# Kernel tuning notes

Measured on AMD Instinct MI355X. Metric: run time of the kernel, lower is better.

The kernel has to match this reference:

```python
import jax, jax.numpy as jnp
import numpy as np

N0, N1, N2 = 100000, 20000, 4000
E1, E2 = 500000, 100000
F_IN, H, C = 512, 512, 10


def setup_inputs() -> dict:
    key = jax.random.key(0)
    ks = jax.random.split(key, 16)
    s = 0.02  # weight scale
    return {
        "x": jax.random.normal(ks[0], (N0, F_IN), jnp.float32),
        "src1": jax.random.randint(ks[1], (E1,), 0, N0),
        "dst1": jax.random.randint(ks[2], (E1,), 0, N1),
        "src2": jax.random.randint(ks[3], (E2,), 0, N1),
        "dst2": jax.random.randint(ks[4], (E2,), 0, N2),
        "Wrel1": jax.random.normal(ks[5], (F_IN, H), jnp.float32) * s,
        "brel1": jax.random.normal(ks[6], (H,), jnp.float32) * s,
        "Wroot1": jax.random.normal(ks[7], (F_IN, H), jnp.float32) * s,
        "Wrel2": jax.random.normal(ks[8], (H, H), jnp.float32) * s,
        "brel2": jax.random.normal(ks[9], (H,), jnp.float32) * s,
        "Wroot2": jax.random.normal(ks[10], (H, H), jnp.float32) * s,
        "Wlin": jax.random.normal(ks[11], (H, H), jnp.float32) * s,
        "blin": jax.random.normal(ks[12], (H,), jnp.float32) * s,
        "Whead": jax.random.normal(ks[13], (H, C), jnp.float32) * s,
        "bhead": jax.random.normal(ks[14], (C,), jnp.float32) * s,
    }


def graph_conv(x_src, x_tgt, src, dst, n_tgt, Wrel, brel, Wroot):
    # PyG GraphConv, aggr='add': lin_rel(sum_j x_src[src_j] -> dst) + lin_root(x_tgt)
    agg = jax.ops.segment_sum(x_src[src], dst, num_segments=n_tgt)
    return agg @ Wrel + brel + x_tgt @ Wroot


def reference(x, src1, dst1, src2, dst2,
              Wrel1, brel1, Wroot1, Wrel2, brel2, Wroot2,
              Wlin, blin, Whead, bhead):
    # Layer 1: [N0, F] -> [N1, H]
    h = graph_conv(x, x[:N1], src1, dst1, N1, Wrel1, brel1, Wroot1)
    h = jax.nn.relu(h)  # dropout is identity in eval mode
    # Layer 2: [N1, H] -> [N2, H]
    h2 = graph_conv(h, h[:N2], src2, dst2, N2, Wrel2, brel2, Wroot2)
    # Dense head
    return (h2 @ Wlin + blin) @ Whead + bhead
```

## Files before the change

kernel.cpp:

```cpp
#include <hip/hip_runtime.h>
#include <hip/hip_bf16.h>
#include <cstdint>


static constexpr int N0 = 100000;
static constexpr int N1 = 20000;
static constexpr int N2 = 4000;
static constexpr int HH = 512;
static constexpr int C  = 10;
static constexpr int M1PAD = 20096;
static constexpr int SLOT = 64;

using frag  = __attribute__((ext_vector_type(8))) short;
using f32x4 = __attribute__((ext_vector_type(4))) float;

__device__ inline float bf2f(unsigned short u) {
    unsigned t = ((unsigned)u) << 16; float f; __builtin_memcpy(&f, &t, 4); return f;
}
__device__ inline unsigned short f2bf(float f) {
    unsigned u; __builtin_memcpy(&u, &f, 4);
    u += 0x7FFFu + ((u >> 16) & 1u);
    return (unsigned short)(u >> 16);
}
__device__ inline void gld16(const void* g, void* l) {
    __builtin_amdgcn_global_load_lds((const __attribute__((address_space(1))) void*)g,
                                     (__attribute__((address_space(3))) void*)l,
                                     16, 0, 0);
}

__global__ __launch_bounds__(256)
void prep1_k(const int* __restrict__ src1, const int* __restrict__ dst1,
             const int* __restrict__ src2, const int* __restrict__ dst2,
             int* __restrict__ cnt1, int* __restrict__ cnt2,
             int* __restrict__ eidx1, int* __restrict__ eidx2,
             int E1, int E2,
             const float* __restrict__ x, unsigned short* __restrict__ xb,
             const float* __restrict__ Wrel1, const float* __restrict__ Wroot1,
             unsigned short* __restrict__ Wt,
             const float* __restrict__ Wlin, const float* __restrict__ Whead,
             float* __restrict__ P1,
             int epb) {
    __shared__ float sh[5120];
    int b = blockIdx.x;
    const int tid = threadIdx.x;
    if (b < 20) {
        for (int i = tid; i < HH * C; i += 256) sh[i] = Whead[i];
        __syncthreads();
        int g = b * 256 + tid;
        int k = g / C, c = g % C;
        const float4* rp = (const float4*)(Wlin + (size_t)k * HH);
        float a0 = 0.f, a1 = 0.f, a2 = 0.f, a3 = 0.f;
#pragma unroll 4
        for (int j = 0; j < HH / 4; ++j) {
            float4 v = rp[j];
            int j4 = j * 4;
            a0 += v.x * sh[(j4    ) * C + c];
            a1 += v.y * sh[(j4 + 1) * C + c];
            a2 += v.z * sh[(j4 + 2) * C + c];
            a3 += v.w * sh[(j4 + 3) * C + c];
        }
        P1[g] = (a0 + a1) + (a2 + a3);
        return;
    }
    b -= 20;
    if (b < 512) {
        int z = b >> 8, rem = b & 255;
        int bx = (rem & 15) * 32, by = (rem >> 4) * 32;
        const float* W = z ? Wroot1 : Wrel1;
        unsigned short* O = Wt + (size_t)z * HH * HH;
        int tx = tid & 31, ty = tid >> 5;
#pragma unroll
        for (int i = 0; i < 4; ++i)
            sh[(ty + i * 8) * 33 + tx] = W[(size_t)(by + ty + i * 8) * HH + bx + tx];
        __syncthreads();
#pragma unroll
        for (int i = 0; i < 4; ++i)
            O[(size_t)(bx + ty + i * 8) * HH + by + tx] = f2bf(sh[tx * 33 + ty + i * 8]);
        return;
    }
    b -= 512;
    {
        int eg = b * epb + tid;
        bool hasE = (tid < epb) && (eg < E1 + E2);
        if (hasE) {
            if (eg < E1) {
                int d = dst1[eg];
                int pos = atomicAdd(&cnt1[d], 1);
                if (pos < SLOT) eidx1[d * SLOT + pos] = src1[eg];
            } else {
                int g2 = eg - E1;
                int d = dst2[g2];
                int pos = atomicAdd(&cnt2[d], 1);
                if (pos < SLOT) eidx2[d * SLOT + pos] = src2[g2];
            }
        }
        int g = b * 256 + tid;
        const float4* p = (const float4*)x + (size_t)g * 4;
        float4 v0 = p[0], v1 = p[1], v2 = p[2], v3 = p[3];
        unsigned short t[16] = {f2bf(v0.x), f2bf(v0.y), f2bf(v0.z), f2bf(v0.w),
                                f2bf(v1.x), f2bf(v1.y), f2bf(v1.z), f2bf(v1.w),
                                f2bf(v2.x), f2bf(v2.y), f2bf(v2.z), f2bf(v2.w),
                                f2bf(v3.x), f2bf(v3.y), f2bf(v3.z), f2bf(v3.w)};
        uint4* o = (uint4*)(xb + (size_t)g * 16);
        o[0] = ((const uint4*)t)[0];
        o[1] = ((const uint4*)t)[1];
    }
}

__global__ __launch_bounds__(1024)
void prep2_k(const float* __restrict__ Wrel2, const float* __restrict__ Wroot2,
             const float* __restrict__ P1,
             const float* __restrict__ brel2, const float* __restrict__ blin,
             const float* __restrict__ Whead, const float* __restrict__ bhead,
             float* __restrict__ W2aT, float* __restrict__ W2bT,
             float* __restrict__ bout) {
    __shared__ float fsh[5120];
    int blk = blockIdx.x;
    int t = threadIdx.x;
    if (blk < 10) {
        for (int i = t; i < HH * C; i += 1024) fsh[i] = P1[i];
        __syncthreads();
        int z = blk >= 5;
        int g = (blk - z * 5) * 1024 + t;
        if (g < HH * C) {
            const float* W = z ? Wroot2 : Wrel2;
            float* O = z ? W2bT : W2aT;
            int k = g / C, c = g % C;
            const float4* rp = (const float4*)(W + (size_t)k * HH);
            float a0 = 0.f, a1 = 0.f, a2 = 0.f, a3 = 0.f;
#pragma unroll 4
            for (int j = 0; j < HH / 4; ++j) {
                float4 v = rp[j];
                int j4 = j * 4;
                a0 += v.x * fsh[(j4    ) * C + c];
                a1 += v.y * fsh[(j4 + 1) * C + c];
                a2 += v.z * fsh[(j4 + 2) * C + c];
                a3 += v.w * fsh[(j4 + 3) * C + c];
            }
            O[c * HH + k] = (a0 + a1) + (a2 + a3);
        }
        return;
    }
    {
        float pr[C];
#pragma unroll
        for (int c = 0; c < C; ++c) pr[c] = 0.f;
        if (t < HH) {
            float br = brel2[t], bl = blin[t];
            const float* p1r = P1 + (size_t)t * C;
            const float* whr = Whead + (size_t)t * C;
#pragma unroll
            for (int c = 0; c < C; ++c) pr[c] = br * p1r[c] + bl * whr[c];
        }
#pragma unroll
        for (int c = 0; c < C; ++c)
#pragma unroll
            for (int off = 32; off; off >>= 1) pr[c] += __shfl_xor(pr[c], off);
        int wv = t >> 6, ln = t & 63;
        if (ln == 0)
#pragma unroll
            for (int c = 0; c < C; ++c) fsh[wv * C + c] = pr[c];
        __syncthreads();
        if (t < C) {
            float acc = bhead[t];
#pragma unroll
            for (int w = 0; w < 16; ++w) acc += fsh[w * C + t];
            bout[t] = acc;
        }
    }
}

__global__ __launch_bounds__(256)
void agg_bf16_k(const unsigned short* __restrict__ x, const int* __restrict__ cnt,
                const int* __restrict__ eidx, unsigned short* __restrict__ out, int n) {
    int node = blockIdx.x * 4 + (threadIdx.x >> 6);
    if (node >= n) return;
    int l = threadIdx.x & 63;
    int deg = min(cnt[node], SLOT);
    const int* ep = eidx + (size_t)node * SLOT;
    int acc[8] = {};
    int i = 0;
    for (; i + 8 <= deg; i += 8) {
        uint4 v[8];
#pragma unroll
        for (int u = 0; u < 8; ++u)
            v[u] = *(const uint4*)(x + (size_t)ep[i + u] * HH + l * 8);
#pragma unroll
        for (int u = 0; u < 8; ++u) {
            const unsigned short* pv = (const unsigned short*)&v[u];
#pragma unroll
            for (int j = 0; j < 8; ++j) acc[j] += (int)(bf2f(pv[j]) * 1048576.0f);
        }
    }
    for (; i < deg; ++i) {
        uint4 a = *(const uint4*)(x + (size_t)ep[i] * HH + l * 8);
        const unsigned short* pa = (const unsigned short*)&a;
#pragma unroll
        for (int j = 0; j < 8; ++j) acc[j] += (int)(bf2f(pa[j]) * 1048576.0f);
    }
    unsigned short o[8];
#pragma unroll
    for (int j = 0; j < 8; ++j)
        o[j] = f2bf((float)acc[j] * (1.0f / 1048576.0f));
    *(uint4*)(out + (size_t)node * HH + l * 8) = *(const uint4*)o;
}

__global__ __launch_bounds__(256)
void gemm_mfma_k(const short* __restrict__ A1, const short* __restrict__ B1t,
                 const short* __restrict__ A2, const short* __restrict__ B2t,
                 const float* __restrict__ bias, unsigned short* __restrict__ Cout,
                 int M) {
    __shared__ __align__(16) short Ls[4 * 128 * 32];
    short* As1 = Ls;
    short* As2 = Ls + 4096;
    short* Bs1 = Ls + 8192;
    short* Bs2 = Ls + 12288;
    const int bn = blockIdx.x * 128;
    const int bm = blockIdx.y * 128;
    const int tid = threadIdx.x;
    const int lane = tid & 63;
    const int wave = tid >> 6;
    const int l15 = lane & 15;
    const int quad = lane >> 4;
    const int wm = (wave >> 1) * 64;
    const int wn = (wave & 1) * 64;
    const int r0 = tid >> 2;
    const int sg = (tid & 3) * 8;

    f32x4 acc[4][4] = {};

    for (int k0 = 0; k0 < 512; k0 += 32) {
        gld16(A1 + (size_t)(bm + r0) * 512 + k0 + sg,        As1 + tid * 8);
        gld16(A1 + (size_t)(bm + r0 + 64) * 512 + k0 + sg,   As1 + (tid + 256) * 8);
        gld16(A2 + (size_t)(bm + r0) * 512 + k0 + sg,        As2 + tid * 8);
        gld16(A2 + (size_t)(bm + r0 + 64) * 512 + k0 + sg,   As2 + (tid + 256) * 8);
        gld16(B1t + (size_t)(bn + r0) * 512 + k0 + sg,       Bs1 + tid * 8);
        gld16(B1t + (size_t)(bn + r0 + 64) * 512 + k0 + sg,  Bs1 + (tid + 256) * 8);
        gld16(B2t + (size_t)(bn + r0) * 512 + k0 + sg,       Bs2 + tid * 8);
        gld16(B2t + (size_t)(bn + r0 + 64) * 512 + k0 + sg,  Bs2 + (tid + 256) * 8);
        __syncthreads();
        {
            frag a[4], b[4];
#pragma unroll
            for (int mi = 0; mi < 4; ++mi)
                a[mi] = *(const frag*)(As1 + (wm + mi * 16 + l15) * 32 + quad * 8);
#pragma unroll
            for (int ni = 0; ni < 4; ++ni)
                b[ni] = *(const frag*)(Bs1 + (wn + ni * 16 + l15) * 32 + quad * 8);
#pragma unroll
            for (int mi = 0; mi < 4; ++mi)
#pragma unroll
                for (int ni = 0; ni < 4; ++ni)
                    acc[mi][ni] = __builtin_amdgcn_mfma_f32_16x16x32_bf16(
                        a[mi], b[ni], acc[mi][ni], 0, 0, 0);
#pragma unroll
            for (int mi = 0; mi < 4; ++mi)
                a[mi] = *(const frag*)(As2 + (wm + mi * 16 + l15) * 32 + quad * 8);
#pragma unroll
            for (int ni = 0; ni < 4; ++ni)
                b[ni] = *(const frag*)(Bs2 + (wn + ni * 16 + l15) * 32 + quad * 8);
#pragma unroll
            for (int mi = 0; mi < 4; ++mi)
#pragma unroll
                for (int ni = 0; ni < 4; ++ni)
                    acc[mi][ni] = __builtin_amdgcn_mfma_f32_16x16x32_bf16(
                        a[mi], b[ni], acc[mi][ni], 0, 0, 0);
        }
        __syncthreads();
    }

#pragma unroll
    for (int ni = 0; ni < 4; ++ni) {
        const int gn = bn + wn + ni * 16 + l15;
        const float bv = bias[gn];
#pragma unroll
        for (int mi = 0; mi < 4; ++mi) {
            const int gm0 = bm + wm + mi * 16 + quad * 4;
#pragma unroll
            for (int r = 0; r < 4; ++r) {
                const int gm = gm0 + r;
                if (gm < M) {
                    float v = fmaxf(acc[mi][ni][r] + bv, 0.f);
                    Cout[(size_t)gm * 512 + gn] = f2bf(v);
                }
            }
        }
    }
}

__global__ __launch_bounds__(256)
void proj_k(const unsigned short* __restrict__ h,
            const float* __restrict__ W2aT, const float* __restrict__ W2bT,
            int* __restrict__ ui, float* __restrict__ vf) {
    int node = blockIdx.x * 4 + (threadIdx.x >> 6);
    if (node >= N1) return;
    int l = threadIdx.x & 63;
    uint4 a = *(const uint4*)(h + (size_t)node * HH + l * 8);
    const unsigned short* pa = (const unsigned short*)&a;
    float r[8];
#pragma unroll
    for (int j = 0; j < 8; ++j) r[j] = bf2f(pa[j]);
#pragma unroll
    for (int c = 0; c < C; ++c) {
        const float* wa = W2aT + c * HH + l * 8;
        float4 w0 = *(const float4*)wa, w1 = *(const float4*)(wa + 4);
        float v = r[0] * w0.x + r[1] * w0.y + r[2] * w0.z + r[3] * w0.w
                + r[4] * w1.x + r[5] * w1.y + r[6] * w1.z + r[7] * w1.w;
#pragma unroll
        for (int off = 32; off; off >>= 1) v += __shfl_xor(v, off);
        if (l == 0) ui[node * C + c] = (int)(v * 4194304.0f);
    }
    if (node < N2) {
#pragma unroll
        for (int c = 0; c < C; ++c) {
            const float* wb = W2bT + c * HH + l * 8;
            float4 w0 = *(const float4*)wb, w1 = *(const float4*)(wb + 4);
            float v = r[0] * w0.x + r[1] * w0.y + r[2] * w0.z + r[3] * w0.w
                    + r[4] * w1.x + r[5] * w1.y + r[6] * w1.z + r[7] * w1.w;
#pragma unroll
            for (int off = 32; off; off >>= 1) v += __shfl_xor(v, off);
            if (l == 0) vf[node * C + c] = v;
        }
    }
}

__global__ __launch_bounds__(256)
void tail2_k(const int* __restrict__ cnt2, const int* __restrict__ eidx2,
             const int* __restrict__ ui, const float* __restrict__ vf,
             const float* __restrict__ bout, float* __restrict__ out) {
    if (threadIdx.x >= 250) return;
    int t = blockIdx.x * 250 + threadIdx.x;
    if (t >= N2 * C) return;
    int n = t / C;
    int c = t - n * C;
    int deg = min(cnt2[n], SLOT);
    const int* ep = eidx2 + (size_t)n * SLOT;
    int acc = 0;
    int i = 0;
    for (; i + 4 <= deg; i += 4) {
        int j0 = ep[i], j1 = ep[i + 1], j2 = ep[i + 2], j3 = ep[i + 3];
        acc += ui[j0 * C + c] + ui[j1 * C + c] + ui[j2 * C + c] + ui[j3 * C + c];
    }
    for (; i < deg; ++i) acc += ui[ep[i] * C + c];
    out[t] = (float)acc * (1.0f / 4194304.0f) + vf[t] + bout[c];
}

extern "C" void kernel_launch(void* const* d_in, const int* in_sizes, int n_in,
                              void* d_out, int out_size, void* d_ws, size_t ws_size,
                              hipStream_t stream) {
    const float* x      = (const float*)d_in[0];
    const int*   src1   = (const int*)d_in[1];
    const int*   dst1   = (const int*)d_in[2];
    const int*   src2   = (const int*)d_in[3];
    const int*   dst2   = (const int*)d_in[4];
    const float* Wrel1  = (const float*)d_in[5];
    const float* brel1  = (const float*)d_in[6];
    const float* Wroot1 = (const float*)d_in[7];
    const float* Wrel2  = (const float*)d_in[8];
    const float* brel2  = (const float*)d_in[9];
    const float* Wroot2 = (const float*)d_in[10];
    const float* Wlin   = (const float*)d_in[11];
    const float* blin   = (const float*)d_in[12];
    const float* Whead  = (const float*)d_in[13];
    const float* bhead  = (const float*)d_in[14];
    float* out = (float*)d_out;

    const int E1 = in_sizes[1];
    const int E2 = in_sizes[3];

    char* w = (char*)d_ws;
    auto alloc = [&](size_t bytes) { char* p = w; w += (bytes + 255) & ~(size_t)255; return p; };
    unsigned short* xb    = (unsigned short*)alloc((size_t)N0 * HH * 2);
    unsigned short* agg1b = (unsigned short*)alloc((size_t)M1PAD * HH * 2);
    unsigned short* hb    = (unsigned short*)alloc((size_t)M1PAD * HH * 2);
    unsigned short* Wt    = (unsigned short*)alloc((size_t)2 * HH * HH * 2);
    float* P1    = (float*)alloc((size_t)HH * C * 4);
    float* W2aT  = (float*)alloc((size_t)HH * C * 4);
    float* W2bT  = (float*)alloc((size_t)HH * C * 4);
    float* boutp = (float*)alloc(256);
    int*   ui    = (int*)alloc((size_t)N1 * C * 4);
    float* vf    = (float*)alloc((size_t)N2 * C * 4);
    int* cnt1  = (int*)alloc((size_t)(N1 + N2) * 4);
    int* cnt2  = cnt1 + N1;
    int* eidx1 = (int*)alloc((size_t)N1 * SLOT * 4);
    int* eidx2 = (int*)alloc((size_t)N2 * SLOT * 4);

    const short* Wrel1t  = (const short*)(Wt);
    const short* Wroot1t = (const short*)(Wt + (size_t)HH * HH);

    hipMemsetAsync(cnt1, 0, (size_t)(N1 + N2) * sizeof(int), stream);

    const int nbCast = N0 * HH / 16 / 256;
    const int epb    = (E1 + E2 + nbCast - 1) / nbCast;
    prep1_k<<<20 + 512 + nbCast, 256, 0, stream>>>(
        src1, dst1, src2, dst2, cnt1, cnt2, eidx1, eidx2, E1, E2,
        x, xb, Wrel1, Wroot1, Wt, Wlin, Whead, P1, epb);

    prep2_k<<<11, 1024, 0, stream>>>(Wrel2, Wroot2, P1,
                                     brel2, blin, Whead, bhead, W2aT, W2bT, boutp);

    agg_bf16_k<<<(N1 + 3) / 4, 256, 0, stream>>>(xb, cnt1, eidx1, agg1b, N1);
    {
        dim3 grid(HH / 128, M1PAD / 128);
        gemm_mfma_k<<<grid, 256, 0, stream>>>(
            (const short*)agg1b, Wrel1t, (const short*)xb, Wroot1t, brel1, hb, N1);
    }

    proj_k<<<(N1 + 3) / 4, 256, 0, stream>>>(hb, W2aT, W2bT, ui, vf);

    tail2_k<<<(N2 * C + 249) / 250, 256, 0, stream>>>(cnt2, eidx2, ui, vf, boutp, out);
}
```

Before: 503.5 us.

## Fuse layer-2 projection into GEMM epilogue and merge prep kernels

```diff
diff --git a/kernel.cpp b/kernel.cpp
--- a/kernel.cpp
+++ b/kernel.cpp
@@ -10,6 +10,8 @@
 static constexpr int C  = 10;
 static constexpr int M1PAD = 20096;
 static constexpr int SLOT = 64;
+static constexpr float FIX = 4194304.0f;
+static constexpr float FIXINV = 1.0f / 4194304.0f;
 
 using frag  = __attribute__((ext_vector_type(8))) short;
 using f32x4 = __attribute__((ext_vector_type(4))) float;
@@ -37,32 +39,96 @@
              const float* __restrict__ x, unsigned short* __restrict__ xb,
              const float* __restrict__ Wrel1, const float* __restrict__ Wroot1,
              unsigned short* __restrict__ Wt,
+             const float* __restrict__ Wrel2, const float* __restrict__ Wroot2,
              const float* __restrict__ Wlin, const float* __restrict__ Whead,
-             float* __restrict__ P1,
+             const float* __restrict__ brel2, const float* __restrict__ blin,
+             const float* __restrict__ bhead,
+             float* __restrict__ W2aT, float* __restrict__ W2bT,
+             float* __restrict__ bout,
              int epb) {
     __shared__ float sh[5120];
     int b = blockIdx.x;
     const int tid = threadIdx.x;
-    if (b < 20) {
+    if (b < 9) {
         for (int i = tid; i < HH * C; i += 256) sh[i] = Whead[i];
         __syncthreads();
-        int g = b * 256 + tid;
-        int k = g / C, c = g % C;
-        const float4* rp = (const float4*)(Wlin + (size_t)k * HH);
-        float a0 = 0.f, a1 = 0.f, a2 = 0.f, a3 = 0.f;
-#pragma unroll 4
-        for (int j = 0; j < HH / 4; ++j) {
-            float4 v = rp[j];
-            int j4 = j * 4;
-            a0 += v.x * sh[(j4    ) * C + c];
-            a1 += v.y * sh[(j4 + 1) * C + c];
-            a2 += v.z * sh[(j4 + 2) * C + c];
-            a3 += v.w * sh[(j4 + 3) * C + c];
-        }
-        P1[g] = (a0 + a1) + (a2 + a3);
+        float p1r[2][C];
+#pragma unroll
+        for (int rr = 0; rr < 2; ++rr) {
+            int j = tid + rr * 256;
+            const float4* wl = (const float4*)(Wlin + (size_t)j * HH);
+            float a[C];
+#pragma unroll
+            for (int c = 0; c < C; ++c) a[c] = 0.f;
+            for (int m4 = 0; m4 < HH / 4; ++m4) {
+                float4 v = wl[m4];
+                int m = m4 * 4;
+#pragma unroll
+                for (int c = 0; c < C; ++c)
+                    a[c] += v.x * sh[m * C + c] + v.y * sh[(m + 1) * C + c]
+                          + v.z * sh[(m + 2) * C + c] + v.w * sh[(m + 3) * C + c];
+            }
+#pragma unroll
+            for (int c = 0; c < C; ++c) p1r[rr][c] = a[c];
+        }
+        __syncthreads();
+#pragma unroll
+        for (int rr = 0; rr < 2; ++rr)
+#pragma unroll
+            for (int c = 0; c < C; ++c) sh[(tid + rr * 256) * C + c] = p1r[rr][c];
+        __syncthreads();
+        if (b < 8) {
+            int z = b >> 2;
+            int k = (b & 3) * 128 + (tid >> 1);
+            int c0 = (tid & 1) * 5;
+            const float* W = z ? Wroot2 : Wrel2;
+            float* O = z ? W2bT : W2aT;
+            const float4* wr = (const float4*)(W + (size_t)k * HH);
+            float a[5] = {};
+            for (int j4 = 0; j4 < HH / 4; ++j4) {
+                float4 v = wr[j4];
+                int j = j4 * 4;
+#pragma unroll
+                for (int cc = 0; cc < 5; ++cc) {
+                    int c = c0 + cc;
+                    a[cc] += v.x * sh[j * C + c] + v.y * sh[(j + 1) * C + c]
+                           + v.z * sh[(j + 2) * C + c] + v.w * sh[(j + 3) * C + c];
+                }
+            }
+#pragma unroll
+            for (int cc = 0; cc < 5; ++cc) O[(c0 + cc) * HH + k] = a[cc];
+        } else {
+            float pr[C];
+#pragma unroll
+            for (int c = 0; c < C; ++c) pr[c] = 0.f;
+#pragma unroll
+            for (int rr = 0; rr < 2; ++rr) {
+                int j = tid + rr * 256;
+                float br = brel2[j], bl = blin[j];
+#pragma unroll
+                for (int c = 0; c < C; ++c)
+                    pr[c] += br * sh[j * C + c] + bl * Whead[j * C + c];
+            }
+#pragma unroll
+            for (int c = 0; c < C; ++c)
+#pragma unroll
+                for (int off = 32; off; off >>= 1) pr[c] += __shfl_xor(pr[c], off);
+            __syncthreads();
+            int wv = tid >> 6, ln = tid & 63;
+            if (ln == 0)
+#pragma unroll
+                for (int c = 0; c < C; ++c) sh[wv * C + c] = pr[c];
+            __syncthreads();
+            if (tid < C) {
+                float acc = bhead[tid];
+#pragma unroll
+                for (int w = 0; w < 4; ++w) acc += sh[w * C + tid];
+                bout[tid] = acc;
+            }
+        }
         return;
     }
-    b -= 20;
+    b -= 9;
     if (b < 512) {
         int z = b >> 8, rem = b & 255;
         int bx = (rem & 15) * 32, by = (rem >> 4) * 32;
@@ -107,69 +173,6 @@
     }
 }
 
-__global__ __launch_bounds__(1024)
-void prep2_k(const float* __restrict__ Wrel2, const float* __restrict__ Wroot2,
-             const float* __restrict__ P1,
-             const float* __restrict__ brel2, const float* __restrict__ blin,
-             const float* __restrict__ Whead, const float* __restrict__ bhead,
-             float* __restrict__ W2aT, float* __restrict__ W2bT,
-             float* __restrict__ bout) {
-    __shared__ float fsh[5120];
-    int blk = blockIdx.x;
-    int t = threadIdx.x;
-    if (blk < 10) {
-        for (int i = t; i < HH * C; i += 1024) fsh[i] = P1[i];
-        __syncthreads();
-        int z = blk >= 5;
-        int g = (blk - z * 5) * 1024 + t;
-        if (g < HH * C) {
-            const float* W = z ? Wroot2 : Wrel2;
-            float* O = z ? W2bT : W2aT;
-            int k = g / C, c = g % C;
-            const float4* rp = (const float4*)(W + (size_t)k * HH);
-            float a0 = 0.f, a1 = 0.f, a2 = 0.f, a3 = 0.f;
-#pragma unroll 4
-            for (int j = 0; j < HH / 4; ++j) {
-                float4 v = rp[j];
-                int j4 = j * 4;
-                a0 += v.x * fsh[(j4    ) * C + c];
-                a1 += v.y * fsh[(j4 + 1) * C + c];
-                a2 += v.z * fsh[(j4 + 2) * C + c];
-                a3 += v.w * fsh[(j4 + 3) * C + c];
-            }
-            O[c * HH + k] = (a0 + a1) + (a2 + a3);
-        }
-        return;
-    }
-    {
-        float pr[C];
-#pragma unroll
-        for (int c = 0; c < C; ++c) pr[c] = 0.f;
-        if (t < HH) {
-            float br = brel2[t], bl = blin[t];
-            const float* p1r = P1 + (size_t)t * C;
-            const float* whr = Whead + (size_t)t * C;
-#pragma unroll
-            for (int c = 0; c < C; ++c) pr[c] = br * p1r[c] + bl * whr[c];
-        }
-#pragma unroll
-        for (int c = 0; c < C; ++c)
-#pragma unroll
-            for (int off = 32; off; off >>= 1) pr[c] += __shfl_xor(pr[c], off);
-        int wv = t >> 6, ln = t & 63;
-        if (ln == 0)
-#pragma unroll
-            for (int c = 0; c < C; ++c) fsh[wv * C + c] = pr[c];
-        __syncthreads();
-        if (t < C) {
-            float acc = bhead[t];
-#pragma unroll
-            for (int w = 0; w < 16; ++w) acc += fsh[w * C + t];
-            bout[t] = acc;
-        }
-    }
-}
-
 __global__ __launch_bounds__(256)
 void agg_bf16_k(const unsigned short* __restrict__ x, const int* __restrict__ cnt,
                 const int* __restrict__ eidx, unsigned short* __restrict__ out, int n) {
@@ -208,9 +211,11 @@
 __global__ __launch_bounds__(256)
 void gemm_mfma_k(const short* __restrict__ A1, const short* __restrict__ B1t,
                  const short* __restrict__ A2, const short* __restrict__ B2t,
-                 const float* __restrict__ bias, unsigned short* __restrict__ Cout,
-                 int M) {
+                 const float* __restrict__ bias,
+                 const float* __restrict__ W2aT, const float* __restrict__ W2bT,
+                 int* __restrict__ uA, int* __restrict__ vA) {
     __shared__ __align__(16) short Ls[4 * 128 * 32];
+    __shared__ float wshA[C * 128], wshB[C * 128];
     short* As1 = Ls;
     short* As2 = Ls + 4096;
     short* Bs1 = Ls + 8192;
@@ -227,6 +232,12 @@
     const int r0 = tid >> 2;
     const int sg = (tid & 3) * 8;
 
+    for (int i = tid; i < C * 128; i += 256) {
+        int c = i >> 7, k = i & 127;
+        wshA[i] = W2aT[c * HH + bn + k];
+        wshB[i] = W2bT[c * HH + bn + k];
+    }
+
     f32x4 acc[4][4] = {};
 
     for (int k0 = 0; k0 < 512; k0 += 32) {
@@ -271,78 +282,83 @@
 
 #pragma unroll
     for (int ni = 0; ni < 4; ++ni) {
-        const int gn = bn + wn + ni * 16 + l15;
-        const float bv = bias[gn];
+        const int lc = wn + ni * 16 + l15;
+        const float bv = bias[bn + lc];
 #pragma unroll
         for (int mi = 0; mi < 4; ++mi) {
-            const int gm0 = bm + wm + mi * 16 + quad * 4;
-#pragma unroll
-            for (int r = 0; r < 4; ++r) {
-                const int gm = gm0 + r;
-                if (gm < M) {
-                    float v = fmaxf(acc[mi][ni][r] + bv, 0.f);
-                    Cout[(size_t)gm * 512 + gn] = f2bf(v);
-                }
-            }
-        }
-    }
-}
-
-__global__ __launch_bounds__(256)
-void proj_k(const unsigned short* __restrict__ h,
-            const float* __restrict__ W2aT, const float* __restrict__ W2bT,
-            int* __restrict__ ui, float* __restrict__ vf) {
-    int node = blockIdx.x * 4 + (threadIdx.x >> 6);
-    if (node >= N1) return;
-    int l = threadIdx.x & 63;
-    uint4 a = *(const uint4*)(h + (size_t)node * HH + l * 8);
-    const unsigned short* pa = (const unsigned short*)&a;
-    float r[8];
-#pragma unroll
-    for (int j = 0; j < 8; ++j) r[j] = bf2f(pa[j]);
-#pragma unroll
-    for (int c = 0; c < C; ++c) {
-        const float* wa = W2aT + c * HH + l * 8;
-        float4 w0 = *(const float4*)wa, w1 = *(const float4*)(wa + 4);
-        float v = r[0] * w0.x + r[1] * w0.y + r[2] * w0.z + r[3] * w0.w
-                + r[4] * w1.x + r[5] * w1.y + r[6] * w1.z + r[7] * w1.w;
-#pragma unroll
-        for (int off = 32; off; off >>= 1) v += __shfl_xor(v, off);
-        if (l == 0) ui[node * C + c] = (int)(v * 4194304.0f);
-    }
-    if (node < N2) {
+            const int lr0 = wm + mi * 16 + quad * 4;
+#pragma unroll
+            for (int r = 0; r < 4; ++r)
+                Ls[(lr0 + r) * 128 + lc] = (short)f2bf(fmaxf(acc[mi][ni][r] + bv, 0.f));
+        }
+    }
+    __syncthreads();
+
+    const int lr = tid >> 1;
+    const int half = tid & 1;
+    const int gm = bm + lr;
+    const bool doV = (gm < N2);
+    float pu[C], pv[C];
+#pragma unroll
+    for (int c = 0; c < C; ++c) { pu[c] = 0.f; pv[c] = 0.f; }
+    const uint4* hrow = (const uint4*)(Ls + lr * 128 + half * 64);
+    for (int ch = 0; ch < 8; ++ch) {
+        uint4 hv = hrow[ch];
+        const unsigned short* ph = (const unsigned short*)&hv;
+        float f[8];
+#pragma unroll
+        for (int j = 0; j < 8; ++j) f[j] = bf2f(ph[j]);
+        const int cb = half * 64 + ch * 8;
 #pragma unroll
         for (int c = 0; c < C; ++c) {
-            const float* wb = W2bT + c * HH + l * 8;
-            float4 w0 = *(const float4*)wb, w1 = *(const float4*)(wb + 4);
-            float v = r[0] * w0.x + r[1] * w0.y + r[2] * w0.z + r[3] * w0.w
-                    + r[4] * w1.x + r[5] * w1.y + r[6] * w1.z + r[7] * w1.w;
-#pragma unroll
-            for (int off = 32; off; off >>= 1) v += __shfl_xor(v, off);
-            if (l == 0) vf[node * C + c] = v;
+            const float* wa = &wshA[c * 128 + cb];
+            float4 w0 = *(const float4*)wa, w1 = *(const float4*)(wa + 4);
+            pu[c] += f[0] * w0.x + f[1] * w0.y + f[2] * w0.z + f[3] * w0.w
+                   + f[4] * w1.x + f[5] * w1.y + f[6] * w1.z + f[7] * w1.w;
+        }
+        if (doV) {
+#pragma unroll
+            for (int c = 0; c < C; ++c) {
+                const float* wb = &wshB[c * 128 + cb];
+                float4 w0 = *(const float4*)wb, w1 = *(const float4*)(wb + 4);
+                pv[c] += f[0] * w0.x + f[1] * w0.y + f[2] * w0.z + f[3] * w0.w
+                       + f[4] * w1.x + f[5] * w1.y + f[6] * w1.z + f[7] * w1.w;
+            }
+        }
+    }
+#pragma unroll
+    for (int c = 0; c < C; ++c) pu[c] += __shfl_xor(pu[c], 1);
+#pragma unroll
+    for (int c = 0; c < C; ++c) pv[c] += __shfl_xor(pv[c], 1);
+    if (half == 0 && gm < N1) {
+        int* up = uA + ((size_t)blockIdx.x * N1 + gm) * C;
+#pragma unroll
+        for (int c = 0; c < C; ++c) up[c] = (int)(pu[c] * FIX);
+        if (doV) {
+            int* vp = vA + ((size_t)blockIdx.x * N2 + gm) * C;
+#pragma unroll
+            for (int c = 0; c < C; ++c) vp[c] = (int)(pv[c] * FIX);
         }
     }
 }
 
 __global__ __launch_bounds__(256)
 void tail2_k(const int* __restrict__ cnt2, const int* __restrict__ eidx2,
-             const int* __restrict__ ui, const float* __restrict__ vf,
+             const int* __restrict__ uA, const int* __restrict__ vA,
              const float* __restrict__ bout, float* __restrict__ out) {
-    if (threadIdx.x >= 250) return;
-    int t = blockIdx.x * 250 + threadIdx.x;
+    int t = blockIdx.x * 256 + threadIdx.x;
     if (t >= N2 * C) return;
     int n = t / C;
     int c = t - n * C;
     int deg = min(cnt2[n], SLOT);
     const int* ep = eidx2 + (size_t)n * SLOT;
     int acc = 0;
-    int i = 0;
-    for (; i + 4 <= deg; i += 4) {
-        int j0 = ep[i], j1 = ep[i + 1], j2 = ep[i + 2], j3 = ep[i + 3];
-        acc += ui[j0 * C + c] + ui[j1 * C + c] + ui[j2 * C + c] + ui[j3 * C + c];
-    }
-    for (; i < deg; ++i) acc += ui[ep[i] * C + c];
-    out[t] = (float)acc * (1.0f / 4194304.0f) + vf[t] + bout[c];
+    for (int i = 0; i < deg; ++i) {
+        int j = ep[i] * C + c;
+        acc += uA[j] + uA[N1 * C + j] + uA[2 * N1 * C + j] + uA[3 * N1 * C + j];
+    }
+    int vacc = vA[t] + vA[N2 * C + t] + vA[2 * N2 * C + t] + vA[3 * N2 * C + t];
+    out[t] = (float)acc * FIXINV + (float)vacc * FIXINV + bout[c];
 }
 
 extern "C" void kernel_launch(void* const* d_in, const int* in_sizes, int n_in,
@@ -372,14 +388,12 @@
     auto alloc = [&](size_t bytes) { char* p = w; w += (bytes + 255) & ~(size_t)255; return p; };
     unsigned short* xb    = (unsigned short*)alloc((size_t)N0 * HH * 2);
     unsigned short* agg1b = (unsigned short*)alloc((size_t)M1PAD * HH * 2);
-    unsigned short* hb    = (unsigned short*)alloc((size_t)M1PAD * HH * 2);
     unsigned short* Wt    = (unsigned short*)alloc((size_t)2 * HH * HH * 2);
-    float* P1    = (float*)alloc((size_t)HH * C * 4);
     float* W2aT  = (float*)alloc((size_t)HH * C * 4);
     float* W2bT  = (float*)alloc((size_t)HH * C * 4);
     float* boutp = (float*)alloc(256);
-    int*   ui    = (int*)alloc((size_t)N1 * C * 4);
-    float* vf    = (float*)alloc((size_t)N2 * C * 4);
+    int*   uA    = (int*)alloc((size_t)4 * N1 * C * 4);
+    int*   vA    = (int*)alloc((size_t)4 * N2 * C * 4);
     int* cnt1  = (int*)alloc((size_t)(N1 + N2) * 4);
     int* cnt2  = cnt1 + N1;
     int* eidx1 = (int*)alloc((size_t)N1 * SLOT * 4);
@@ -392,21 +406,19 @@
 
     const int nbCast = N0 * HH / 16 / 256;
     const int epb    = (E1 + E2 + nbCast - 1) / nbCast;
-    prep1_k<<<20 + 512 + nbCast, 256, 0, stream>>>(
+    prep1_k<<<9 + 512 + nbCast, 256, 0, stream>>>(
         src1, dst1, src2, dst2, cnt1, cnt2, eidx1, eidx2, E1, E2,
-        x, xb, Wrel1, Wroot1, Wt, Wlin, Whead, P1, epb);
-
-    prep2_k<<<11, 1024, 0, stream>>>(Wrel2, Wroot2, P1,
-                                     brel2, blin, Whead, bhead, W2aT, W2bT, boutp);
+        x, xb, Wrel1, Wroot1, Wt, Wrel2, Wroot2, Wlin, Whead,
+        brel2, blin, bhead, W2aT, W2bT, boutp, epb);
 
     agg_bf16_k<<<(N1 + 3) / 4, 256, 0, stream>>>(xb, cnt1, eidx1, agg1b, N1);
+
     {
         dim3 grid(HH / 128, M1PAD / 128);
         gemm_mfma_k<<<grid, 256, 0, stream>>>(
-            (const short*)agg1b, Wrel1t, (const short*)xb, Wroot1t, brel1, hb, N1);
-    }
-
-    proj_k<<<(N1 + 3) / 4, 256, 0, stream>>>(hb, W2aT, W2bT, ui, vf);
-
-    tail2_k<<<(N2 * C + 249) / 250, 256, 0, stream>>>(cnt2, eidx2, ui, vf, boutp, out);
-}
+            (const short*)agg1b, Wrel1t, (const short*)xb, Wroot1t, brel1,
+            W2aT, W2bT, uA, vA);
+    }
+
+    tail2_k<<<(N2 * C + 255) / 256, 256, 0, stream>>>(cnt2, eidx2, uA, vA, boutp, out);
+}
```

After: 537.5 us. +6.7%, slower.

## Fuse layer-2 projection into GEMM epilogue, drop h materialization and proj kernel

Applied to the files above, without the earlier changes.

```diff
diff --git a/kernel.cpp b/kernel.cpp
--- a/kernel.cpp
+++ b/kernel.cpp
@@ -10,6 +10,8 @@
 static constexpr int C  = 10;
 static constexpr int M1PAD = 20096;
 static constexpr int SLOT = 64;
+static constexpr float FIX = 4194304.0f;
+static constexpr float FIXINV = 1.0f / 4194304.0f;
 
 using frag  = __attribute__((ext_vector_type(8))) short;
 using f32x4 = __attribute__((ext_vector_type(4))) float;
@@ -208,9 +210,11 @@
 __global__ __launch_bounds__(256)
 void gemm_mfma_k(const short* __restrict__ A1, const short* __restrict__ B1t,
                  const short* __restrict__ A2, const short* __restrict__ B2t,
-                 const float* __restrict__ bias, unsigned short* __restrict__ Cout,
-                 int M) {
+                 const float* __restrict__ bias,
+                 const float* __restrict__ W2aT, const float* __restrict__ W2bT,
+                 int* __restrict__ uA, int* __restrict__ vA) {
     __shared__ __align__(16) short Ls[4 * 128 * 32];
+    __shared__ float wshA[C * 128], wshB[C * 128];
     short* As1 = Ls;
     short* As2 = Ls + 4096;
     short* Bs1 = Ls + 8192;
@@ -227,6 +231,12 @@
     const int r0 = tid >> 2;
     const int sg = (tid & 3) * 8;
 
+    for (int i = tid; i < C * 128; i += 256) {
+        int c = i >> 7, k = i & 127;
+        wshA[i] = W2aT[c * HH + bn + k];
+        wshB[i] = W2bT[c * HH + bn + k];
+    }
+
     f32x4 acc[4][4] = {};
 
     for (int k0 = 0; k0 < 512; k0 += 32) {
@@ -271,78 +281,83 @@
 
 #pragma unroll
     for (int ni = 0; ni < 4; ++ni) {
-        const int gn = bn + wn + ni * 16 + l15;
-        const float bv = bias[gn];
+        const int lc = wn + ni * 16 + l15;
+        const float bv = bias[bn + lc];
 #pragma unroll
         for (int mi = 0; mi < 4; ++mi) {
-            const int gm0 = bm + wm + mi * 16 + quad * 4;
-#pragma unroll
-            for (int r = 0; r < 4; ++r) {
-                const int gm = gm0 + r;
-                if (gm < M) {
-                    float v = fmaxf(acc[mi][ni][r] + bv, 0.f);
-                    Cout[(size_t)gm * 512 + gn] = f2bf(v);
-                }
+            const int lr0 = wm + mi * 16 + quad * 4;
+#pragma unroll
+            for (int r = 0; r < 4; ++r)
+                Ls[(lr0 + r) * 128 + lc] = (short)f2bf(fmaxf(acc[mi][ni][r] + bv, 0.f));
+        }
+    }
+    __syncthreads();
+
+    const int lr = tid >> 1;
+    const int half = tid & 1;
+    const int gm = bm + lr;
+    const bool doV = (gm < N2);
+    float pu[C], pv[C];
+#pragma unroll
+    for (int c = 0; c < C; ++c) { pu[c] = 0.f; pv[c] = 0.f; }
+    const uint4* hrow = (const uint4*)(Ls + lr * 128 + half * 64);
+    for (int ch = 0; ch < 8; ++ch) {
+        uint4 hv = hrow[ch];
+        const unsigned short* ph = (const unsigned short*)&hv;
+        float f[8];
+#pragma unroll
+        for (int j = 0; j < 8; ++j) f[j] = bf2f(ph[j]);
+        const int cb = half * 64 + ch * 8;
+#pragma unroll
+        for (int c = 0; c < C; ++c) {
+            const float* wa = &wshA[c * 128 + cb];
+            float4 w0 = *(const float4*)wa, w1 = *(const float4*)(wa + 4);
+            pu[c] += f[0] * w0.x + f[1] * w0.y + f[2] * w0.z + f[3] * w0.w
+                   + f[4] * w1.x + f[5] * w1.y + f[6] * w1.z + f[7] * w1.w;
+        }
+        if (doV) {
+#pragma unroll
+            for (int c = 0; c < C; ++c) {
+                const float* wb = &wshB[c * 128 + cb];
+                float4 w0 = *(const float4*)wb, w1 = *(const float4*)(wb + 4);
+                pv[c] += f[0] * w0.x + f[1] * w0.y + f[2] * w0.z + f[3] * w0.w
+                       + f[4] * w1.x + f[5] * w1.y + f[6] * w1.z + f[7] * w1.w;
             }
         }
     }
-}
-
-__global__ __launch_bounds__(256)
-void proj_k(const unsigned short* __restrict__ h,
-            const float* __restrict__ W2aT, const float* __restrict__ W2bT,
-            int* __restrict__ ui, float* __restrict__ vf) {
-    int node = blockIdx.x * 4 + (threadIdx.x >> 6);
-    if (node >= N1) return;
-    int l = threadIdx.x & 63;
-    uint4 a = *(const uint4*)(h + (size_t)node * HH + l * 8);
-    const unsigned short* pa = (const unsigned short*)&a;
-    float r[8];
-#pragma unroll
-    for (int j = 0; j < 8; ++j) r[j] = bf2f(pa[j]);
-#pragma unroll
-    for (int c = 0; c < C; ++c) {
-        const float* wa = W2aT + c * HH + l * 8;
-        float4 w0 = *(const float4*)wa, w1 = *(const float4*)(wa + 4);
-        float v = r[0] * w0.x + r[1] * w0.y + r[2] * w0.z + r[3] * w0.w
-                + r[4] * w1.x + r[5] * w1.y + r[6] * w1.z + r[7] * w1.w;
-#pragma unroll
-        for (int off = 32; off; off >>= 1) v += __shfl_xor(v, off);
-        if (l == 0) ui[node * C + c] = (int)(v * 4194304.0f);
-    }
-    if (node < N2) {
-#pragma unroll
-        for (int c = 0; c < C; ++c) {
-            const float* wb = W2bT + c * HH + l * 8;
-            float4 w0 = *(const float4*)wb, w1 = *(const float4*)(wb + 4);
-            float v = r[0] * w0.x + r[1] * w0.y + r[2] * w0.z + r[3] * w0.w
-                    + r[4] * w1.x + r[5] * w1.y + r[6] * w1.z + r[7] * w1.w;
-#pragma unroll
-            for (int off = 32; off; off >>= 1) v += __shfl_xor(v, off);
-            if (l == 0) vf[node * C + c] = v;
+#pragma unroll
+    for (int c = 0; c < C; ++c) pu[c] += __shfl_xor(pu[c], 1);
+#pragma unroll
+    for (int c = 0; c < C; ++c) pv[c] += __shfl_xor(pv[c], 1);
+    if (half == 0 && gm < N1) {
+        int* up = uA + ((size_t)blockIdx.x * N1 + gm) * C;
+#pragma unroll
+        for (int c = 0; c < C; ++c) up[c] = (int)(pu[c] * FIX);
+        if (doV) {
+            int* vp = vA + ((size_t)blockIdx.x * N2 + gm) * C;
+#pragma unroll
+            for (int c = 0; c < C; ++c) vp[c] = (int)(pv[c] * FIX);
         }
     }
 }
 
 __global__ __launch_bounds__(256)
 void tail2_k(const int* __restrict__ cnt2, const int* __restrict__ eidx2,
-             const int* __restrict__ ui, const float* __restrict__ vf,
+             const int* __restrict__ uA, const int* __restrict__ vA,
              const float* __restrict__ bout, float* __restrict__ out) {
-    if (threadIdx.x >= 250) return;
-    int t = blockIdx.x * 250 + threadIdx.x;
+    int t = blockIdx.x * 256 + threadIdx.x;
     if (t >= N2 * C) return;
     int n = t / C;
     int c = t - n * C;
     int deg = min(cnt2[n], SLOT);
     const int* ep = eidx2 + (size_t)n * SLOT;
     int acc = 0;
-    int i = 0;
-    for (; i + 4 <= deg; i += 4) {
-        int j0 = ep[i], j1 = ep[i + 1], j2 = ep[i + 2], j3 = ep[i + 3];
-        acc += ui[j0 * C + c] + ui[j1 * C + c] + ui[j2 * C + c] + ui[j3 * C + c];
-    }
-    for (; i < deg; ++i) acc += ui[ep[i] * C + c];
-    out[t] = (float)acc * (1.0f / 4194304.0f) + vf[t] + bout[c];
+    for (int i = 0; i < deg; ++i) {
+        int j = ep[i] * C + c;
+        acc += uA[j] + uA[N1 * C + j] + uA[2 * N1 * C + j] + uA[3 * N1 * C + j];
+    }
+    int vacc = vA[t] + vA[N2 * C + t] + vA[2 * N2 * C + t] + vA[3 * N2 * C + t];
+    out[t] = (float)acc * FIXINV + (float)vacc * FIXINV + bout[c];
 }
 
 extern "C" void kernel_launch(void* const* d_in, const int* in_sizes, int n_in,
@@ -372,14 +387,13 @@
     auto alloc = [&](size_t bytes) { char* p = w; w += (bytes + 255) & ~(size_t)255; return p; };
     unsigned short* xb    = (unsigned short*)alloc((size_t)N0 * HH * 2);
     unsigned short* agg1b = (unsigned short*)alloc((size_t)M1PAD * HH * 2);
-    unsigned short* hb    = (unsigned short*)alloc((size_t)M1PAD * HH * 2);
     unsigned short* Wt    = (unsigned short*)alloc((size_t)2 * HH * HH * 2);
     float* P1    = (float*)alloc((size_t)HH * C * 4);
     float* W2aT  = (float*)alloc((size_t)HH * C * 4);
     float* W2bT  = (float*)alloc((size_t)HH * C * 4);
     float* boutp = (float*)alloc(256);
-    int*   ui    = (int*)alloc((size_t)N1 * C * 4);
-    float* vf    = (float*)alloc((size_t)N2 * C * 4);
+    int*   uA    = (int*)alloc((size_t)4 * N1 * C * 4);
+    int*   vA    = (int*)alloc((size_t)4 * N2 * C * 4);
     int* cnt1  = (int*)alloc((size_t)(N1 + N2) * 4);
     int* cnt2  = cnt1 + N1;
     int* eidx1 = (int*)alloc((size_t)N1 * SLOT * 4);
@@ -400,13 +414,13 @@
                                      brel2, blin, Whead, bhead, W2aT, W2bT, boutp);
 
     agg_bf16_k<<<(N1 + 3) / 4, 256, 0, stream>>>(xb, cnt1, eidx1, agg1b, N1);
+
     {
         dim3 grid(HH / 128, M1PAD / 128);
         gemm_mfma_k<<<grid, 256, 0, stream>>>(
-            (const short*)agg1b, Wrel1t, (const short*)xb, Wroot1t, brel1, hb, N1);
-    }
-
-    proj_k<<<(N1 + 3) / 4, 256, 0, stream>>>(hb, W2aT, W2bT, ui, vf);
-
-    tail2_k<<<(N2 * C + 249) / 250, 256, 0, stream>>>(cnt2, eidx2, ui, vf, boutp, out);
-}
+            (const short*)agg1b, Wrel1t, (const short*)xb, Wroot1t, brel1,
+            W2aT, W2bT, uA, vA);
+    }
+
+    tail2_k<<<(N2 * C + 255) / 256, 256, 0, stream>>>(cnt2, eidx2, uA, vA, boutp, out);
+}
```

Measured after the change: 499.3 us. No clear change (-0.8%).
